# Kernel tuning notes

Measured on AMD Instinct MI355X. Metric: run time of the kernel, lower is better.

Reference implementation:

```python
import jax, jax.numpy as jnp
import numpy as np
from jax import lax

EPS = 1e-6  # LayerNorm2d eps


def _ln2d(x, w, b):
    # channel-wise LayerNorm over dim 1 of [B,C,H,W]
    mu = jnp.mean(x, axis=1, keepdims=True)
    var = jnp.mean((x - mu) ** 2, axis=1, keepdims=True)
    return (x - mu) / jnp.sqrt(var + EPS) * w[None, :, None, None] + b[None, :, None, None]


def _conv1x1(x, w, b):
    # w: [O, C]
    return jnp.einsum('bchw,oc->bohw', x, w) + b[None, :, None, None]


def _dconv(x, w, b):
    # 3x3 conv, dilation 4, padding 4 -> same H,W. w: [O, C, 3, 3]
    y = lax.conv_general_dilated(x, w, window_strides=(1, 1),
                                 padding=((4, 4), (4, 4)), rhs_dilation=(4, 4),
                                 dimension_numbers=('NCHW', 'OIHW', 'NCHW'))
    return y + b[None, :, None, None]


def _forward(x_l, x_r, nl_w, nl_b, nr_w, nr_b, lp1_w, lp1_b, rp1_w, rp1_b,
             dl_w, dl_b, dr_w, dr_b, lp2_w, lp2_b, rp2_w, rp2_b, beta, gamma):
    c = x_l.shape[1]
    scale = c ** (-0.5)
    N_l = _ln2d(x_l, nl_w, nl_b)
    N_r = _ln2d(x_r, nr_w, nr_b)
    V_l = jnp.transpose(_conv1x1(x_l, lp2_w, lp2_b), (0, 2, 3, 1))   # [B,H,W,C]
    V_r = jnp.transpose(_conv1x1(x_r, rp2_w, rp2_b), (0, 2, 3, 1))
    Q_l = jnp.transpose(_conv1x1(N_l, lp1_w, lp1_b), (0, 2, 3, 1))   # [B,H,W,C]
    Q_r = jnp.transpose(_conv1x1(N_r, rp1_w, rp1_b), (0, 2, 3, 1))
    K_l_T = jnp.transpose(_dconv(N_l, dl_w, dl_b), (0, 2, 1, 3))     # [B,H,C,W]
    K_r_T = jnp.transpose(_dconv(N_r, dr_w, dr_b), (0, 2, 1, 3))
    # per-row cross attention: [B,H,W,W]
    attn_r2l = jnp.einsum('bhwc,bhcv->bhwv', Q_l, K_r_T) * scale
    attn_l2r = jnp.einsum('bhwc,bhcv->bhwv', Q_r, K_l_T) * scale
    F_r2l = jnp.einsum('bhwv,bhvc->bhwc', jax.nn.softmax(attn_r2l, axis=-1), V_r)
    F_l2r = jnp.einsum('bhwv,bhvc->bhwc', jax.nn.softmax(attn_l2r, axis=-1), V_l)
    F_r2l = jnp.transpose(F_r2l, (0, 3, 1, 2)) * beta   # [B,C,H,W]
    F_l2r = jnp.transpose(F_l2r, (0, 3, 1, 2)) * gamma
    return x_l + F_r2l, x_r + F_l2r


def setup_inputs() -> dict:
    key = jax.random.key(0)
    ks = jax.random.split(key, 12)
    B, C, H, W = 2, 128, 192, 512
    s = 0.02
    rn = lambda k, shp: s * jax.random.normal(k, shp, jnp.float32)
    return {
        'x_l': jax.random.normal(ks[0], (B, C, H, W), jnp.float32),
        'x_r': jax.random.normal(ks[1], (B, C, H, W), jnp.float32),
        'nl_w': jnp.ones((C,), jnp.float32), 'nl_b': jnp.zeros((C,), jnp.float32),
        'nr_w': jnp.ones((C,), jnp.float32), 'nr_b': jnp.zeros((C,), jnp.float32),
        'lp1_w': rn(ks[2], (C, C)), 'lp1_b': jnp.zeros((C,), jnp.float32),
        'rp1_w': rn(ks[3], (C, C)), 'rp1_b': jnp.zeros((C,), jnp.float32),
        'dl_w': rn(ks[4], (C, C, 3, 3)), 'dl_b': jnp.zeros((C,), jnp.float32),
        'dr_w': rn(ks[5], (C, C, 3, 3)), 'dr_b': jnp.zeros((C,), jnp.float32),
        'lp2_w': rn(ks[6], (C, C)), 'lp2_b': jnp.zeros((C,), jnp.float32),
        'rp2_w': rn(ks[7], (C, C)), 'rp2_b': jnp.zeros((C,), jnp.float32),
        'beta': 0.1 * jax.random.normal(ks[8], (1, C, 1, 1), jnp.float32),
        'gamma': 0.1 * jax.random.normal(ks[9], (1, C, 1, 1), jnp.float32),
    }


def reference(x_l, x_r, nl_w, nl_b, nr_w, nr_b, lp1_w, lp1_b, rp1_w, rp1_b,
              dl_w, dl_b, dr_w, dr_b, lp2_w, lp2_b, rp2_w, rp2_b, beta, gamma):
    return _forward(x_l, x_r, nl_w, nl_b, nr_w, nr_b, lp1_w, lp1_b, rp1_w, rp1_b,
                    dl_w, dl_b, dr_w, dr_b, lp2_w, lp2_b, rp2_w, rp2_b, beta, gamma)
```

## Files before the change

### kernel.cpp

```cpp
#include <hip/hip_runtime.h>
#include <stdint.h>

#define CC 128
#define HH 192
#define WW 512
#define BB 2
#define HW (HH*WW)
#define CHW (CC*HW)
#define TENS (BB*CHW)

typedef __attribute__((ext_vector_type(8))) short bf16x8;
typedef __attribute__((ext_vector_type(4))) short bf16x4;
typedef __attribute__((ext_vector_type(4))) float f32x4;

__device__ __forceinline__ unsigned short f2bf(float f) {
    union { float f; unsigned u; } v; v.f = f;
    return (unsigned short)((v.u + 0x7FFFu + ((v.u >> 16) & 1u)) >> 16);
}
__device__ __forceinline__ float bf2f(unsigned short u) {
    union { unsigned u; float f; } v; v.u = ((unsigned)u) << 16;
    return v.f;
}
__device__ __forceinline__ uint32_t cvtpk(float lo, float hi) {
    uint32_t r;
    asm("v_cvt_pk_bf16_f32 %0, %1, %2" : "=v"(r) : "v"(lo), "v"(hi));
    return r;
}
__device__ __forceinline__ f32x4 MFMA(bf16x8 a, bf16x8 b, f32x4 c) {
    return __builtin_amdgcn_mfma_f32_16x16x32_bf16(a, b, c, 0, 0, 0);
}
__device__ __forceinline__ f32x4 MFMA16(bf16x4 a, bf16x4 b, f32x4 c) {
#if __has_builtin(__builtin_amdgcn_mfma_f32_16x16x16_bf16)
    return __builtin_amdgcn_mfma_f32_16x16x16_bf16(a, b, c, 0, 0, 0);
#elif __has_builtin(__builtin_amdgcn_mfma_f32_16x16x16bf16_1k)
    return __builtin_amdgcn_mfma_f32_16x16x16bf16_1k(a, b, c, 0, 0, 0);
#else
    f32x4 d = c;
    asm("v_mfma_f32_16x16x16_bf16 %0, %1, %2, %0" : "+v"(d) : "v"(a), "v"(b));
    return d;
#endif
}
__device__ __forceinline__ void gload_lds16(const void* g, void* l) {
    __builtin_amdgcn_global_load_lds(
        (const __attribute__((address_space(1))) void*)g,
        (__attribute__((address_space(3))) void*)l, 16, 0, 0);
}

__global__ __launch_bounds__(256) void wcast_k(
    const float* __restrict__ dlw, const float* __restrict__ drw,
    unsigned short* __restrict__ wd)
{
    int i = blockIdx.x * 256 + threadIdx.x;
    if (i >= 2 * 9 * CC * CC) return;
    int e  = i & 7;
    int l  = (i >> 3) & 63;
    int n_ = (i >> 9) & 3;
    int kk = (i >> 11) & 3;
    int oh = (i >> 13) & 1;
    int rest = i >> 14;
    int tap = rest % 9;
    int side = rest / 9;
    int o = oh * 64 + n_ * 16 + (l & 15);
    int c = kk * 32 + (l >> 4) * 8 + e;
    const float* src = side ? drw : dlw;
    wd[i] = f2bf(src[((size_t)o * CC + c) * 9 + tap]);
}

__global__ __launch_bounds__(256) void lnv_k(
    const float* __restrict__ xl, const float* __restrict__ xr,
    const float* __restrict__ nlw, const float* __restrict__ nlb,
    const float* __restrict__ nrw, const float* __restrict__ nrb,
    const float* __restrict__ wlp, const float* __restrict__ blp,
    const float* __restrict__ wrp, const float* __restrict__ brp,
    unsigned short* __restrict__ ntl, unsigned short* __restrict__ ntr,
    unsigned short* __restrict__ vlo, unsigned short* __restrict__ vro)
{
    const int side = blockIdx.y;
    const float* x  = side ? xr : xl;
    const float* nw = side ? nrw : nlw;
    const float* nb = side ? nrb : nlb;
    const float* wv = side ? wrp : wlp;
    const float* bv = side ? brp : blp;
    unsigned short* nt = side ? ntr : ntl;
    unsigned short* vo = side ? vro : vlo;
    const int bid = blockIdx.x;
    const int wt = bid & 7, h = (bid >> 3) % HH, b = bid / (8 * HH);
    const int w0 = wt * 64;
    const int t = threadIdx.x;

    __shared__ unsigned short sA[64][136];
    __shared__ unsigned short sB[128][136];
    __shared__ float red[8][64];
    __shared__ float smu[64], srs[64];

    {
        const int w = t & 63, cg = t >> 6;
        const float* xp = x + (size_t)b * CHW + (size_t)h * WW + w0 + w;
        float s = 0.f, q = 0.f;
        for (int i = 0; i < 16; i++) {
            int c = cg * 32 + i * 2;
            float v0 = xp[(size_t)c * HW];
            float v1 = xp[(size_t)(c + 1) * HW];
            *(uint32_t*)&sA[w][c] = cvtpk(v0, v1);
            s += v0 + v1; q += v0 * v0 + v1 * v1;
        }
        red[cg][w] = s; red[4 + cg][w] = q;
    }
    for (int it = 0; it < 16; it++) {
        int f = it * 1024 + t * 4;
        int o = f >> 7, c = f & 127;
        float4 v = *(const float4*)(wv + o * CC + c);
        *(uint32_t*)&sB[o][c]     = cvtpk(v.x, v.y);
        *(uint32_t*)&sB[o][c + 2] = cvtpk(v.z, v.w);
    }
    __syncthreads();
    if (t < 64) {
        float S = red[0][t] + red[1][t] + red[2][t] + red[3][t];
        float Q = red[4][t] + red[5][t] + red[6][t] + red[7][t];
        float mu = S * (1.f / CC);
        float var = fmaxf(Q * (1.f / CC) - mu * mu, 0.f);
        smu[t] = mu; srs[t] = rsqrtf(var + 1e-6f);
    }
    __syncthreads();
    {
        const int cl = (t & 63) * 2, wg = t >> 6;
        const float nwa = nw[cl], nwb = nw[cl + 1];
        const float nba = nb[cl], nbb = nb[cl + 1];
        unsigned short* npb = nt + ((size_t)(b * HH + h) * WW + w0) * CC;
        for (int wp = 0; wp < 16; wp++) {
            int w = wp * 4 + wg;
            float mu = smu[w], rs = srs[w];
            float v0 = (bf2f(sA[w][cl]) - mu) * rs * nwa + nba;
            float v1 = (bf2f(sA[w][cl + 1]) - mu) * rs * nwb + nbb;
            *(uint32_t*)&npb[(size_t)w * CC + cl] = cvtpk(v0, v1);
        }
    }
    const int wid = t >> 6, l = t & 63, lr = l & 15, lg = l >> 4;
    f32x4 acc[8] = {};
    for (int kk = 0; kk < 4; kk++) {
        bf16x8 a = *(const bf16x8*)&sA[wid * 16 + lr][kk * 32 + lg * 8];
#pragma unroll
        for (int n_ = 0; n_ < 8; n_++) {
            bf16x8 bb = *(const bf16x8*)&sB[n_ * 16 + lr][kk * 32 + lg * 8];
            acc[n_] = MFMA(a, bb, acc[n_]);
        }
    }
    unsigned short* vp = vo + ((size_t)(b * HH + h) * CC) * WW + w0;
    for (int n_ = 0; n_ < 8; n_++) {
        int o = n_ * 16 + lr;
        float bias = bv[o];
        uint2 uu;
        uu.x = cvtpk(acc[n_][0] + bias, acc[n_][1] + bias);
        uu.y = cvtpk(acc[n_][2] + bias, acc[n_][3] + bias);
        *(uint2*)&vp[(size_t)o * WW + wid * 16 + lg * 4] = uu;
    }
}

__global__ __launch_bounds__(256) void dconv_k(
    const unsigned short* __restrict__ ntl, const unsigned short* __restrict__ ntr,
    const unsigned short* __restrict__ wfr,
    const float* __restrict__ dlb, const float* __restrict__ drb,
    unsigned short* __restrict__ klo, unsigned short* __restrict__ kro)
{
    const int side = blockIdx.y;
    const unsigned short* nt = side ? ntr : ntl;
    const unsigned short* wbase = wfr + (size_t)side * 9 * 16384;
    const float* bd = side ? drb : dlb;
    unsigned short* ko = side ? kro : klo;
    const int bid0 = blockIdx.x;
    const int lgc = (bid0 & 7) * 192 + (bid0 >> 3);
    const int wt = lgc & 3;
    const int hb = lgc >> 2;
    const int h = hb % HH, b = hb / HH;
    const int w0 = wt * 128;
    const int t = threadIdx.x;
    const int wid = t >> 6, l = t & 63, lr = l & 15, lg = l >> 4;
    const int whalf = wid & 1, ohalf = wid >> 1;

    __shared__ unsigned short sA[136][136];

    f32x4 acc[4][4] = {};
    for (int dy = 0; dy < 3; dy++) {
        const int hh = h + 4 * (dy - 1);
        const bool hok = (hh >= 0 && hh < HH);
        __syncthreads();
        for (int f = t * 8; f < 136 * 128; f += 2048) {
            int wloc = f >> 7, c = f & 127;
            int w = w0 - 4 + wloc;
            bf16x8 v = {0, 0, 0, 0, 0, 0, 0, 0};
            if (hok && w >= 0 && w < WW)
                v = *(const bf16x8*)(nt + ((size_t)(b * HH + hh) * WW + w) * CC + c);
            *(bf16x8*)&sA[wloc][c] = v;
        }
        __syncthreads();
#pragma unroll
        for (int dx = 0; dx < 3; dx++) {
            const unsigned short* wtap =
                wbase + (size_t)(dy * 3 + dx) * 16384 + ohalf * 8192 + l * 8;
#pragma unroll
            for (int kk = 0; kk < 4; kk++) {
                bf16x8 bfr[4];
#pragma unroll
                for (int n_ = 0; n_ < 4; n_++)
                    bfr[n_] = *(const bf16x8*)(wtap + (kk * 4 + n_) * 512);
                bf16x8 af[4];
#pragma unroll
                for (int g = 0; g < 4; g++)
                    af[g] = *(const bf16x8*)&sA[whalf * 64 + g * 16 + lr + 4 * dx][kk * 32 + lg * 8];
#pragma unroll
                for (int g = 0; g < 4; g++)
#pragma unroll
                    for (int n_ = 0; n_ < 4; n_++)
                        acc[g][n_] = MFMA(af[g], bfr[n_], acc[g][n_]);
            }
        }
    }
    unsigned short* kp = ko + ((size_t)(b * HH + h) * WW + w0) * CC;
    for (int g = 0; g < 4; g++)
        for (int n_ = 0; n_ < 4; n_++) {
            int o = ohalf * 64 + n_ * 16 + lr;
            float bias = bd[o];
            for (int j = 0; j < 4; j++) {
                int w = whalf * 64 + g * 16 + lg * 4 + j;
                kp[(size_t)w * CC + o] = f2bf(acc[g][n_][j] + bias);
            }
        }
}

__global__ __launch_bounds__(256, 3) void attn_k(
    const unsigned short* __restrict__ ntl, const unsigned short* __restrict__ ntr,
    const unsigned short* __restrict__ kl,  const unsigned short* __restrict__ kr,
    const unsigned short* __restrict__ vtl, const unsigned short* __restrict__ vtr,
    const float* __restrict__ lp1w, const float* __restrict__ lp1b,
    const float* __restrict__ rp1w, const float* __restrict__ rp1b,
    const float* __restrict__ xl, const float* __restrict__ xr,
    const float* __restrict__ beta, const float* __restrict__ gamma,
    float* __restrict__ out)
{
    __shared__ __align__(16) char smem[52224];
    unsigned short* sQ  = (unsigned short*)smem;
    unsigned short* sWh = (unsigned short*)(smem + 34816);

    const int dir = blockIdx.z;
    const unsigned short* nq  = dir ? ntr : ntl;
    const unsigned short* kws = dir ? kl : kr;
    const unsigned short* vws = dir ? vtl : vtr;
    const float* wq   = dir ? rp1w : lp1w;
    const float* bq   = dir ? rp1b : lp1b;
    const float* xres = dir ? xr : xl;
    const float* mult = dir ? gamma : beta;
    float* op = out + (size_t)dir * TENS;

    const int bid = blockIdx.x;
    const int xcd = bid & 7;
    const int s   = bid >> 3;
    const int qb  = s & 3;
    const int bh  = xcd + 8 * (s >> 2);
    const int q0  = qb * 128;
    const int t = threadIdx.x;
    const int wid = t >> 6, l = t & 63, lr = l & 15, lg = l >> 4;

    const unsigned short* ksrc = kws + (size_t)bh * WW * CC;
    const unsigned short* vsrc = vws + (size_t)bh * CC * WW;

    int koff[4], voff[4];
#pragma unroll
    for (int it = 0; it < 4; it++) {
        int row = it * 16 + wid * 4 + (l >> 4);
        int gci = (l & 15) ^ (row & 7);
        koff[it] = row * CC + gci * 8;
    }
#pragma unroll
    for (int it = 0; it < 4; it++) {
        int row = it * 32 + wid * 8 + (l >> 3);
        int gci = (l & 7) ^ (row & 7);
        voff[it] = row * WW + gci * 8;
    }

    {
        const unsigned short* nsrc = nq + ((size_t)bh * WW + q0) * CC;
        for (int it = 0; it < 8; it++) {
            int f = it * 2048 + t * 8;
            *(bf16x8*)&sQ[(f >> 7) * 136 + (f & 127)] = *(const bf16x8*)(nsrc + f);
        }
        for (int it = 0; it < 8; it++) {
            int f = it * 1024 + t * 4;
            int o = f >> 7, c = f & 127;
            float4 v = *(const float4*)(wq + o * CC + c);
            *(uint32_t*)&sWh[o * 136 + c]     = cvtpk(v.x, v.y);
            *(uint32_t*)&sWh[o * 136 + c + 2] = cvtpk(v.z, v.w);
        }
    }
    f32x4 qacc[2][8] = {};
    __syncthreads();
    for (int kk = 0; kk < 4; kk++) {
        bf16x8 a0 = *(const bf16x8*)&sQ[(wid * 32 + lr) * 136 + kk * 32 + lg * 8];
        bf16x8 a1 = *(const bf16x8*)&sQ[(wid * 32 + 16 + lr) * 136 + kk * 32 + lg * 8];
#pragma unroll
        for (int n_ = 0; n_ < 4; n_++) {
            bf16x8 b = *(const bf16x8*)&sWh[(n_ * 16 + lr) * 136 + kk * 32 + lg * 8];
            qacc[0][n_] = MFMA(a0, b, qacc[0][n_]);
            qacc[1][n_] = MFMA(a1, b, qacc[1][n_]);
        }
    }
    __syncthreads();
    for (int it = 0; it < 8; it++) {
        int f = it * 1024 + t * 4;
        int o = f >> 7, c = f & 127;
        float4 v = *(const float4*)(wq + (o + 64) * CC + c);
        *(uint32_t*)&sWh[o * 136 + c]     = cvtpk(v.x, v.y);
        *(uint32_t*)&sWh[o * 136 + c + 2] = cvtpk(v.z, v.w);
    }
    __syncthreads();
    for (int kk = 0; kk < 4; kk++) {
        bf16x8 a0 = *(const bf16x8*)&sQ[(wid * 32 + lr) * 136 + kk * 32 + lg * 8];
        bf16x8 a1 = *(const bf16x8*)&sQ[(wid * 32 + 16 + lr) * 136 + kk * 32 + lg * 8];
#pragma unroll
        for (int n_ = 0; n_ < 4; n_++) {
            bf16x8 b = *(const bf16x8*)&sWh[(n_ * 16 + lr) * 136 + kk * 32 + lg * 8];
            qacc[0][4 + n_] = MFMA(a0, b, qacc[0][4 + n_]);
            qacc[1][4 + n_] = MFMA(a1, b, qacc[1][4 + n_]);
        }
    }
    __syncthreads();
    {
        const float SCL = 0.08838834764831845f * 1.4426950408889634f;
#pragma unroll
        for (int mg = 0; mg < 2; mg++)
#pragma unroll
            for (int n_ = 0; n_ < 8; n_++) {
                float bias = bq[n_ * 16 + lr];
#pragma unroll
                for (int j = 0; j < 4; j++)
                    sQ[(wid * 32 + mg * 16 + lg * 4 + j) * 136 + n_ * 16 + lr] =
                        f2bf((qacc[mg][n_][j] + bias) * SCL);
            }
    }
    __syncthreads();
    bf16x8 qf[2][4];
#pragma unroll
    for (int qg = 0; qg < 2; qg++)
#pragma unroll
        for (int kk = 0; kk < 4; kk++)
            qf[qg][kk] = *(const bf16x8*)&sQ[(wid * 32 + qg * 16 + lr) * 136 + kk * 32 + lg * 8];

    f32x4 oacc[8][2] = {};
    float mrow[2] = {-1e30f, -1e30f};
    float lrow[2] = {0.f, 0.f};
    const int lr7 = lr & 7;

    for (int kb = 0; kb < 8; kb++) {
        __syncthreads();
        {
            const unsigned short* kS = ksrc + kb * 64 * CC;
            const unsigned short* vS = vsrc + kb * 64;
#pragma unroll
            for (int it = 0; it < 4; it++)
                gload_lds16(kS + koff[it], smem + it * 4096 + wid * 1024);
#pragma unroll
            for (int it = 0; it < 4; it++)
                gload_lds16(vS + voff[it], smem + 16384 + it * 4096 + wid * 1024);
        }
        __syncthreads();
        f32x4 sacc[2][4] = {};
        __builtin_amdgcn_s_setprio(1);
        for (int kk = 0; kk < 4; kk++)
#pragma unroll
            for (int n_ = 0; n_ < 4; n_++) {
                bf16x8 kf = *(const bf16x8*)(smem + (n_ * 16 + lr) * 256
                                             + (((kk * 4 + lg) ^ lr7) << 4));
                sacc[0][n_] = MFMA(kf, qf[0][kk], sacc[0][n_]);
                sacc[1][n_] = MFMA(kf, qf[1][kk], sacc[1][n_]);
            }
        __builtin_amdgcn_s_setprio(0);
        float pm[2];
#pragma unroll
        for (int qg = 0; qg < 2; qg++) {
            float m_ = sacc[qg][0][0];
#pragma unroll
            for (int n_ = 0; n_ < 4; n_++)
#pragma unroll
                for (int j = 0; j < 4; j++) m_ = fmaxf(m_, sacc[qg][n_][j]);
            m_ = fmaxf(m_, __shfl_xor(m_, 16, 64));
            m_ = fmaxf(m_, __shfl_xor(m_, 32, 64));
            pm[qg] = m_;
        }
        bool need = (pm[0] - mrow[0] > 8.f) || (pm[1] - mrow[1] > 8.f);
        if (__any(need)) {
            float al[2];
#pragma unroll
            for (int qg = 0; qg < 2; qg++) {
                float mn = fmaxf(mrow[qg], pm[qg]);
                al[qg] = exp2f(mrow[qg] - mn);
                mrow[qg] = mn;
                lrow[qg] *= al[qg];
            }
#pragma unroll
            for (int n_ = 0; n_ < 8; n_++)
#pragma unroll
                for (int qg = 0; qg < 2; qg++) {
                    f32x4 o = oacc[n_][qg];
                    o[0] *= al[qg]; o[1] *= al[qg]; o[2] *= al[qg]; o[3] *= al[qg];
                    oacc[n_][qg] = o;
                }
        }
#pragma unroll
        for (int qg = 0; qg < 2; qg++) {
            float rs = 0.f;
#pragma unroll
            for (int n_ = 0; n_ < 4; n_++)
#pragma unroll
                for (int j = 0; j < 4; j++) {
                    float e = exp2f(sacc[qg][n_][j] - mrow[qg]);
                    sacc[qg][n_][j] = e;
                    rs += e;
                }
            rs += __shfl_xor(rs, 16, 64);
            rs += __shfl_xor(rs, 32, 64);
            lrow[qg] += rs;
        }
        __builtin_amdgcn_s_setprio(1);
#pragma unroll
        for (int n_ = 0; n_ < 4; n_++) {
            union { uint32_t u[2]; bf16x4 v; } b0, b1;
            b0.u[0] = cvtpk(sacc[0][n_][0], sacc[0][n_][1]);
            b0.u[1] = cvtpk(sacc[0][n_][2], sacc[0][n_][3]);
            b1.u[0] = cvtpk(sacc[1][n_][0], sacc[1][n_][1]);
            b1.u[1] = cvtpk(sacc[1][n_][2], sacc[1][n_][3]);
#pragma unroll
            for (int n8 = 0; n8 < 8; n8++) {
                bf16x4 va = *(const bf16x4*)(smem + 16384 + (n8 * 16 + lr) * 128
                                             + ((((n_ * 2) + (lg >> 1)) ^ lr7) << 4)
                                             + ((lg & 1) << 3));
                oacc[n8][0] = MFMA16(va, b0.v, oacc[n8][0]);
                oacc[n8][1] = MFMA16(va, b1.v, oacc[n8][1]);
            }
        }
        __builtin_amdgcn_s_setprio(0);
    }

    const float inv0 = 1.f / lrow[0], inv1 = 1.f / lrow[1];
    const int b = bh / HH, h = bh % HH;
    const int w_0 = q0 + wid * 32 + lr;
    const float* xp0 = xres + (size_t)b * CHW + (size_t)h * WW + w_0;
    float* outp0 = op + (size_t)b * CHW + (size_t)h * WW + w_0;
#pragma unroll
    for (int n_ = 0; n_ < 8; n_++) {
        float4 m4 = *(const float4*)&mult[n_ * 16 + lg * 4];
#pragma unroll
        for (int j = 0; j < 4; j++) {
            int c = n_ * 16 + lg * 4 + j;
            float mj = (&m4.x)[j];
            outp0[(size_t)c * HW]      = xp0[(size_t)c * HW]      + oacc[n_][0][j] * inv0 * mj;
            outp0[(size_t)c * HW + 16] = xp0[(size_t)c * HW + 16] + oacc[n_][1][j] * inv1 * mj;
        }
    }
}

extern "C" void kernel_launch(void* const* d_in, const int* in_sizes, int n_in,
                              void* d_out, int out_size, void* d_ws, size_t ws_size,
                              hipStream_t stream)
{
    const float* xl   = (const float*)d_in[0];
    const float* xr   = (const float*)d_in[1];
    const float* nlw  = (const float*)d_in[2];
    const float* nlb  = (const float*)d_in[3];
    const float* nrw  = (const float*)d_in[4];
    const float* nrb  = (const float*)d_in[5];
    const float* lp1w = (const float*)d_in[6];
    const float* lp1b = (const float*)d_in[7];
    const float* rp1w = (const float*)d_in[8];
    const float* rp1b = (const float*)d_in[9];
    const float* dlw  = (const float*)d_in[10];
    const float* dlb  = (const float*)d_in[11];
    const float* drw  = (const float*)d_in[12];
    const float* drb  = (const float*)d_in[13];
    const float* lp2w = (const float*)d_in[14];
    const float* lp2b = (const float*)d_in[15];
    const float* rp2w = (const float*)d_in[16];
    const float* rp2b = (const float*)d_in[17];
    const float* beta = (const float*)d_in[18];
    const float* gamma= (const float*)d_in[19];
    float* out = (float*)d_out;

    unsigned short* ws = (unsigned short*)d_ws;
    const size_t A = (size_t)TENS;
    unsigned short* Ntl = ws;
    unsigned short* Ntr = ws + A;
    unsigned short* Kl  = ws + 2 * A;
    unsigned short* Kr  = ws + 3 * A;
    unsigned short* Vtl = ws + 4 * A;
    unsigned short* Vtr = ws + 5 * A;
    unsigned short* Wd  = ws + 6 * A;

    wcast_k<<<dim3(1152), 256, 0, stream>>>(dlw, drw, Wd);
    lnv_k<<<dim3(3072, 2), 256, 0, stream>>>(xl, xr, nlw, nlb, nrw, nrb,
        lp2w, lp2b, rp2w, rp2b, Ntl, Ntr, Vtl, Vtr);
    dconv_k<<<dim3(1536, 2), 256, 0, stream>>>(Ntl, Ntr, Wd, dlb, drb, Kl, Kr);
    attn_k<<<dim3(1536, 1, 2), 256, 0, stream>>>(Ntl, Ntr, Kl, Kr, Vtl, Vtr,
        lp1w, lp1b, rp1w, rp1b, xl, xr, beta, gamma, out);
}
```

Before: 523.3 us.

## Move Q projection from attention kernel into LayerNorm/V-projection kernel

Computes the scaled Q projection inside lnv_k, reusing the normalized tile already in shared memory, and writes Q to a new workspace buffer. The attention kernel then loads precomputed Q fragments straight from global memory, dropping its weight staging, the two MFMA passes and several barriers. Its shared memory falls from 52 KB to 32 KB, which may allow more resident blocks. The cost is an extra bf16 Q tensor written and read through global memory, plus more work and LDS traffic in lnv_k.

```diff
diff --git a/kernel.cpp b/kernel.cpp
--- a/kernel.cpp
+++ b/kernel.cpp
@@ -72,8 +72,11 @@
     const float* __restrict__ nrw, const float* __restrict__ nrb,
     const float* __restrict__ wlp, const float* __restrict__ blp,
     const float* __restrict__ wrp, const float* __restrict__ brp,
+    const float* __restrict__ wlq, const float* __restrict__ blq,
+    const float* __restrict__ wrq, const float* __restrict__ brq,
     unsigned short* __restrict__ ntl, unsigned short* __restrict__ ntr,
-    unsigned short* __restrict__ vlo, unsigned short* __restrict__ vro)
+    unsigned short* __restrict__ vlo, unsigned short* __restrict__ vro,
+    unsigned short* __restrict__ qlo, unsigned short* __restrict__ qro)
 {
     const int side = blockIdx.y;
     const float* x  = side ? xr : xl;
@@ -81,12 +84,16 @@
     const float* nb = side ? nrb : nlb;
     const float* wv = side ? wrp : wlp;
     const float* bv = side ? brp : blp;
+    const float* wq = side ? wrq : wlq;
+    const float* bq = side ? brq : blq;
     unsigned short* nt = side ? ntr : ntl;
     unsigned short* vo = side ? vro : vlo;
+    unsigned short* qo = side ? qro : qlo;
     const int bid = blockIdx.x;
     const int wt = bid & 7, h = (bid >> 3) % HH, b = bid / (8 * HH);
     const int w0 = wt * 64;
     const int t = threadIdx.x;
+    const int wid = t >> 6, l = t & 63, lr = l & 15, lg = l >> 4;
 
     __shared__ unsigned short sA[64][136];
     __shared__ unsigned short sB[128][136];
@@ -135,7 +142,6 @@
             *(uint32_t*)&npb[(size_t)w * CC + cl] = cvtpk(v0, v1);
         }
     }
-    const int wid = t >> 6, l = t & 63, lr = l & 15, lg = l >> 4;
     f32x4 acc[8] = {};
     for (int kk = 0; kk < 4; kk++) {
         bf16x8 a = *(const bf16x8*)&sA[wid * 16 + lr][kk * 32 + lg * 8];
@@ -153,6 +159,51 @@
         uu.x = cvtpk(acc[n_][0] + bias, acc[n_][1] + bias);
         uu.y = cvtpk(acc[n_][2] + bias, acc[n_][3] + bias);
         *(uint2*)&vp[(size_t)o * WW + wid * 16 + lg * 4] = uu;
+    }
+    __syncthreads();
+    {
+        const int w = wid * 16 + (l >> 2), c0 = (l & 3) * 32;
+        const float mu = smu[w], rs = srs[w];
+        for (int i = 0; i < 32; i += 2) {
+            int c = c0 + i;
+            float v0 = (bf2f(sA[w][c]) - mu) * rs * nw[c] + nb[c];
+            float v1 = (bf2f(sA[w][c + 1]) - mu) * rs * nw[c + 1] + nb[c + 1];
+            *(uint32_t*)&sA[w][c] = cvtpk(v0, v1);
+        }
+    }
+    for (int it = 0; it < 16; it++) {
+        int f = it * 1024 + t * 4;
+        int o = f >> 7, c = f & 127;
+        float4 v = *(const float4*)(wq + o * CC + c);
+        *(uint32_t*)&sB[o][c]     = cvtpk(v.x, v.y);
+        *(uint32_t*)&sB[o][c + 2] = cvtpk(v.z, v.w);
+    }
+    __syncthreads();
+    f32x4 qa[8] = {};
+    for (int kk = 0; kk < 4; kk++) {
+        bf16x8 a = *(const bf16x8*)&sA[wid * 16 + lr][kk * 32 + lg * 8];
+#pragma unroll
+        for (int n_ = 0; n_ < 8; n_++) {
+            bf16x8 bb = *(const bf16x8*)&sB[n_ * 16 + lr][kk * 32 + lg * 8];
+            qa[n_] = MFMA(a, bb, qa[n_]);
+        }
+    }
+    const float SCL = 0.08838834764831845f * 1.4426950408889634f;
+    for (int n_ = 0; n_ < 8; n_++) {
+        int o = n_ * 16 + lr;
+        float bias = bq[o];
+#pragma unroll
+        for (int j = 0; j < 4; j++)
+            sA[wid * 16 + lg * 4 + j][o] = f2bf((qa[n_][j] + bias) * SCL);
+    }
+    {
+        unsigned short* qp = qo + ((size_t)(b * HH + h) * WW + w0 + wid * 16) * CC;
+#pragma unroll
+        for (int r = 0; r < 4; r++) {
+            int row = r * 4 + (l >> 4);
+            int col = (l & 15) * 8;
+            *(bf16x8*)&qp[row * CC + col] = *(const bf16x8*)&sA[wid * 16 + row][col];
+        }
     }
 }
 
@@ -228,25 +279,19 @@
 }
 
 __global__ __launch_bounds__(256, 3) void attn_k(
-    const unsigned short* __restrict__ ntl, const unsigned short* __restrict__ ntr,
+    const unsigned short* __restrict__ qsl, const unsigned short* __restrict__ qsr,
     const unsigned short* __restrict__ kl,  const unsigned short* __restrict__ kr,
     const unsigned short* __restrict__ vtl, const unsigned short* __restrict__ vtr,
-    const float* __restrict__ lp1w, const float* __restrict__ lp1b,
-    const float* __restrict__ rp1w, const float* __restrict__ rp1b,
     const float* __restrict__ xl, const float* __restrict__ xr,
     const float* __restrict__ beta, const float* __restrict__ gamma,
     float* __restrict__ out)
 {
-    __shared__ __align__(16) char smem[52224];
-    unsigned short* sQ  = (unsigned short*)smem;
-    unsigned short* sWh = (unsigned short*)(smem + 34816);
+    __shared__ __align__(16) char smem[32768];
 
     const int dir = blockIdx.z;
-    const unsigned short* nq  = dir ? ntr : ntl;
+    const unsigned short* qws = dir ? qsr : qsl;
     const unsigned short* kws = dir ? kl : kr;
     const unsigned short* vws = dir ? vtl : vtr;
-    const float* wq   = dir ? rp1w : lp1w;
-    const float* bq   = dir ? rp1b : lp1b;
     const float* xres = dir ? xr : xl;
     const float* mult = dir ? gamma : beta;
     float* op = out + (size_t)dir * TENS;
@@ -263,6 +308,17 @@
     const unsigned short* ksrc = kws + (size_t)bh * WW * CC;
     const unsigned short* vsrc = vws + (size_t)bh * CC * WW;
 
+    bf16x8 qf[2][4];
+    {
+        const unsigned short* qsrc = qws + ((size_t)bh * WW + q0) * CC;
+#pragma unroll
+        for (int qg = 0; qg < 2; qg++)
+#pragma unroll
+            for (int kk = 0; kk < 4; kk++)
+                qf[qg][kk] = *(const bf16x8*)(qsrc + (wid * 32 + qg * 16 + lr) * CC
+                                              + kk * 32 + lg * 8);
+    }
+
     int koff[4], voff[4];
 #pragma unroll
     for (int it = 0; it < 4; it++) {
@@ -276,73 +332,6 @@
         int gci = (l & 7) ^ (row & 7);
         voff[it] = row * WW + gci * 8;
     }
-
-    {
-        const unsigned short* nsrc = nq + ((size_t)bh * WW + q0) * CC;
-        for (int it = 0; it < 8; it++) {
-            int f = it * 2048 + t * 8;
-            *(bf16x8*)&sQ[(f >> 7) * 136 + (f & 127)] = *(const bf16x8*)(nsrc + f);
-        }
-        for (int it = 0; it < 8; it++) {
-            int f = it * 1024 + t * 4;
-            int o = f >> 7, c = f & 127;
-            float4 v = *(const float4*)(wq + o * CC + c);
-            *(uint32_t*)&sWh[o * 136 + c]     = cvtpk(v.x, v.y);
-            *(uint32_t*)&sWh[o * 136 + c + 2] = cvtpk(v.z, v.w);
-        }
-    }
-    f32x4 qacc[2][8] = {};
-    __syncthreads();
-    for (int kk = 0; kk < 4; kk++) {
-        bf16x8 a0 = *(const bf16x8*)&sQ[(wid * 32 + lr) * 136 + kk * 32 + lg * 8];
-        bf16x8 a1 = *(const bf16x8*)&sQ[(wid * 32 + 16 + lr) * 136 + kk * 32 + lg * 8];
-#pragma unroll
-        for (int n_ = 0; n_ < 4; n_++) {
-            bf16x8 b = *(const bf16x8*)&sWh[(n_ * 16 + lr) * 136 + kk * 32 + lg * 8];
-            qacc[0][n_] = MFMA(a0, b, qacc[0][n_]);
-            qacc[1][n_] = MFMA(a1, b, qacc[1][n_]);
-        }
-    }
-    __syncthreads();
-    for (int it = 0; it < 8; it++) {
-        int f = it * 1024 + t * 4;
-        int o = f >> 7, c = f & 127;
-        float4 v = *(const float4*)(wq + (o + 64) * CC + c);
-        *(uint32_t*)&sWh[o * 136 + c]     = cvtpk(v.x, v.y);
-        *(uint32_t*)&sWh[o * 136 + c + 2] = cvtpk(v.z, v.w);
-    }
-    __syncthreads();
-    for (int kk = 0; kk < 4; kk++) {
-        bf16x8 a0 = *(const bf16x8*)&sQ[(wid * 32 + lr) * 136 + kk * 32 + lg * 8];
-        bf16x8 a1 = *(const bf16x8*)&sQ[(wid * 32 + 16 + lr) * 136 + kk * 32 + lg * 8];
-#pragma unroll
-        for (int n_ = 0; n_ < 4; n_++) {
-            bf16x8 b = *(const bf16x8*)&sWh[(n_ * 16 + lr) * 136 + kk * 32 + lg * 8];
-            qacc[0][4 + n_] = MFMA(a0, b, qacc[0][4 + n_]);
-            qacc[1][4 + n_] = MFMA(a1, b, qacc[1][4 + n_]);
-        }
-    }
-    __syncthreads();
-    {
-        const float SCL = 0.08838834764831845f * 1.4426950408889634f;
-#pragma unroll
-        for (int mg = 0; mg < 2; mg++)
-#pragma unroll
-            for (int n_ = 0; n_ < 8; n_++) {
-                float bias = bq[n_ * 16 + lr];
-#pragma unroll
-                for (int j = 0; j < 4; j++)
-                    sQ[(wid * 32 + mg * 16 + lg * 4 + j) * 136 + n_ * 16 + lr] =
-                        f2bf((qacc[mg][n_][j] + bias) * SCL);
-            }
-    }
-    __syncthreads();
-    bf16x8 qf[2][4];
-#pragma unroll
-    for (int qg = 0; qg < 2; qg++)
-#pragma unroll
-        for (int kk = 0; kk < 4; kk++)
-            qf[qg][kk] = *(const bf16x8*)&sQ[(wid * 32 + qg * 16 + lr) * 136 + kk * 32 + lg * 8];
 
     f32x4 oacc[8][2] = {};
     float mrow[2] = {-1e30f, -1e30f};
@@ -491,12 +480,15 @@
     unsigned short* Kr  = ws + 3 * A;
     unsigned short* Vtl = ws + 4 * A;
     unsigned short* Vtr = ws + 5 * A;
-    unsigned short* Wd  = ws + 6 * A;
+    unsigned short* Qsl = ws + 6 * A;
+    unsigned short* Qsr = ws + 7 * A;
+    unsigned short* Wd  = ws + 8 * A;
 
     wcast_k<<<dim3(1152), 256, 0, stream>>>(dlw, drw, Wd);
     lnv_k<<<dim3(3072, 2), 256, 0, stream>>>(xl, xr, nlw, nlb, nrw, nrb,
-        lp2w, lp2b, rp2w, rp2b, Ntl, Ntr, Vtl, Vtr);
+        lp2w, lp2b, rp2w, rp2b, lp1w, lp1b, rp1w, rp1b,
+        Ntl, Ntr, Vtl, Vtr, Qsl, Qsr);
     dconv_k<<<dim3(1536, 2), 256, 0, stream>>>(Ntl, Ntr, Wd, dlb, drb, Kl, Kr);
-    attn_k<<<dim3(1536, 1, 2), 256, 0, stream>>>(Ntl, Ntr, Kl, Kr, Vtl, Vtr,
-        lp1w, lp1b, rp1w, rp1b, xl, xr, beta, gamma, out);
-}
+    attn_k<<<dim3(1536, 1, 2), 256, 0, stream>>>(Qsl, Qsr, Kl, Kr, Vtl, Vtr,
+        xl, xr, beta, gamma, out);
+}
```

New measurement: 578.5 us. 10.6% more time.

## Keep projected Q in registers as MFMA B-operand fragments, drop sQ staging

Applied to the files above, without the earlier changes.

The Q projection now computes W·N^T directly, so its accumulator layout matches the B-operand fragment of the 16x16x16 MFMA used in the QK^T score computation. The projected, scaled Q therefore stays in registers and is no longer written to and read back from LDS. This removes the sQ buffer, shrinking LDS from 52KB to 32KB, which could allow more resident blocks, and it removes several barriers. The trade-offs are that the score loop switches from K=32 MFMAs to twice as many K=16 MFMAs with narrower LDS reads, and N is loaded straight from global memory into registers.

```diff
diff --git a/kernel.cpp b/kernel.cpp
--- a/kernel.cpp
+++ b/kernel.cpp
@@ -237,9 +237,8 @@
     const float* __restrict__ beta, const float* __restrict__ gamma,
     float* __restrict__ out)
 {
-    __shared__ __align__(16) char smem[52224];
-    unsigned short* sQ  = (unsigned short*)smem;
-    unsigned short* sWh = (unsigned short*)(smem + 34816);
+    __shared__ __align__(16) char smem[32768];
+    unsigned short* sWh = (unsigned short*)smem;
 
     const int dir = blockIdx.z;
     const unsigned short* nq  = dir ? ntr : ntl;
@@ -263,6 +262,51 @@
     const unsigned short* ksrc = kws + (size_t)bh * WW * CC;
     const unsigned short* vsrc = vws + (size_t)bh * CC * WW;
 
+    bf16x8 nf[2][4];
+    {
+        const unsigned short* nsrc = nq + ((size_t)bh * WW + q0) * CC;
+#pragma unroll
+        for (int qg = 0; qg < 2; qg++)
+#pragma unroll
+            for (int kk = 0; kk < 4; kk++)
+                nf[qg][kk] = *(const bf16x8*)(nsrc + (wid * 32 + qg * 16 + lr) * CC
+                                              + kk * 32 + lg * 8);
+    }
+
+    const float SCL = 0.08838834764831845f * 1.4426950408889634f;
+    uint2 qfb[8][2];
+#pragma unroll
+    for (int h_ = 0; h_ < 2; h_++) {
+        if (h_) __syncthreads();
+        for (int it = 0; it < 8; it++) {
+            int f = it * 1024 + t * 4;
+            int o = f >> 7, c = f & 127;
+            float4 v = *(const float4*)(wq + (h_ * 64 + o) * CC + c);
+            *(uint32_t*)&sWh[o * 136 + c]     = cvtpk(v.x, v.y);
+            *(uint32_t*)&sWh[o * 136 + c + 2] = cvtpk(v.z, v.w);
+        }
+        __syncthreads();
+#pragma unroll
+        for (int n4 = 0; n4 < 4; n4++) {
+            bf16x8 wqA[4];
+#pragma unroll
+            for (int kk = 0; kk < 4; kk++)
+                wqA[kk] = *(const bf16x8*)&sWh[(n4 * 16 + lr) * 136 + kk * 32 + lg * 8];
+            f32x4 qa0 = {}, qa1 = {};
+#pragma unroll
+            for (int kk = 0; kk < 4; kk++) {
+                qa0 = MFMA(wqA[kk], nf[0][kk], qa0);
+                qa1 = MFMA(wqA[kk], nf[1][kk], qa1);
+            }
+            int n_ = h_ * 4 + n4;
+            float4 b4 = *(const float4*)(bq + n_ * 16 + lg * 4);
+            qfb[n_][0].x = cvtpk((qa0[0] + b4.x) * SCL, (qa0[1] + b4.y) * SCL);
+            qfb[n_][0].y = cvtpk((qa0[2] + b4.z) * SCL, (qa0[3] + b4.w) * SCL);
+            qfb[n_][1].x = cvtpk((qa1[0] + b4.x) * SCL, (qa1[1] + b4.y) * SCL);
+            qfb[n_][1].y = cvtpk((qa1[2] + b4.z) * SCL, (qa1[3] + b4.w) * SCL);
+        }
+    }
+
     int koff[4], voff[4];
 #pragma unroll
     for (int it = 0; it < 4; it++) {
@@ -276,73 +320,6 @@
         int gci = (l & 7) ^ (row & 7);
         voff[it] = row * WW + gci * 8;
     }
-
-    {
-        const unsigned short* nsrc = nq + ((size_t)bh * WW + q0) * CC;
-        for (int it = 0; it < 8; it++) {
-            int f = it * 2048 + t * 8;
-            *(bf16x8*)&sQ[(f >> 7) * 136 + (f & 127)] = *(const bf16x8*)(nsrc + f);
-        }
-        for (int it = 0; it < 8; it++) {
-            int f = it * 1024 + t * 4;
-            int o = f >> 7, c = f & 127;
-            float4 v = *(const float4*)(wq + o * CC + c);
-            *(uint32_t*)&sWh[o * 136 + c]     = cvtpk(v.x, v.y);
-            *(uint32_t*)&sWh[o * 136 + c + 2] = cvtpk(v.z, v.w);
-        }
-    }
-    f32x4 qacc[2][8] = {};
-    __syncthreads();
-    for (int kk = 0; kk < 4; kk++) {
-        bf16x8 a0 = *(const bf16x8*)&sQ[(wid * 32 + lr) * 136 + kk * 32 + lg * 8];
-        bf16x8 a1 = *(const bf16x8*)&sQ[(wid * 32 + 16 + lr) * 136 + kk * 32 + lg * 8];
-#pragma unroll
-        for (int n_ = 0; n_ < 4; n_++) {
-            bf16x8 b = *(const bf16x8*)&sWh[(n_ * 16 + lr) * 136 + kk * 32 + lg * 8];
-            qacc[0][n_] = MFMA(a0, b, qacc[0][n_]);
-            qacc[1][n_] = MFMA(a1, b, qacc[1][n_]);
-        }
-    }
-    __syncthreads();
-    for (int it = 0; it < 8; it++) {
-        int f = it * 1024 + t * 4;
-        int o = f >> 7, c = f & 127;
-        float4 v = *(const float4*)(wq + (o + 64) * CC + c);
-        *(uint32_t*)&sWh[o * 136 + c]     = cvtpk(v.x, v.y);
-        *(uint32_t*)&sWh[o * 136 + c + 2] = cvtpk(v.z, v.w);
-    }
-    __syncthreads();
-    for (int kk = 0; kk < 4; kk++) {
-        bf16x8 a0 = *(const bf16x8*)&sQ[(wid * 32 + lr) * 136 + kk * 32 + lg * 8];
-        bf16x8 a1 = *(const bf16x8*)&sQ[(wid * 32 + 16 + lr) * 136 + kk * 32 + lg * 8];
-#pragma unroll
-        for (int n_ = 0; n_ < 4; n_++) {
-            bf16x8 b = *(const bf16x8*)&sWh[(n_ * 16 + lr) * 136 + kk * 32 + lg * 8];
-            qacc[0][4 + n_] = MFMA(a0, b, qacc[0][4 + n_]);
-            qacc[1][4 + n_] = MFMA(a1, b, qacc[1][4 + n_]);
-        }
-    }
-    __syncthreads();
-    {
-        const float SCL = 0.08838834764831845f * 1.4426950408889634f;
-#pragma unroll
-        for (int mg = 0; mg < 2; mg++)
-#pragma unroll
-            for (int n_ = 0; n_ < 8; n_++) {
-                float bias = bq[n_ * 16 + lr];
-#pragma unroll
-                for (int j = 0; j < 4; j++)
-                    sQ[(wid * 32 + mg * 16 + lg * 4 + j) * 136 + n_ * 16 + lr] =
-                        f2bf((qacc[mg][n_][j] + bias) * SCL);
-            }
-    }
-    __syncthreads();
-    bf16x8 qf[2][4];
-#pragma unroll
-    for (int qg = 0; qg < 2; qg++)
-#pragma unroll
-        for (int kk = 0; kk < 4; kk++)
-            qf[qg][kk] = *(const bf16x8*)&sQ[(wid * 32 + qg * 16 + lr) * 136 + kk * 32 + lg * 8];
 
     f32x4 oacc[8][2] = {};
     float mrow[2] = {-1e30f, -1e30f};
@@ -364,14 +341,17 @@
         __syncthreads();
         f32x4 sacc[2][4] = {};
         __builtin_amdgcn_s_setprio(1);
-        for (int kk = 0; kk < 4; kk++)
-#pragma unroll
-            for (int n_ = 0; n_ < 4; n_++) {
-                bf16x8 kf = *(const bf16x8*)(smem + (n_ * 16 + lr) * 256
-                                             + (((kk * 4 + lg) ^ lr7) << 4));
-                sacc[0][n_] = MFMA(kf, qf[0][kk], sacc[0][n_]);
-                sacc[1][n_] = MFMA(kf, qf[1][kk], sacc[1][n_]);
-            }
+#pragma unroll
+        for (int n4 = 0; n4 < 4; n4++) {
+#pragma unroll
+            for (int s_ = 0; s_ < 8; s_++) {
+                bf16x4 ka = *(const bf16x4*)(smem + (n4 * 16 + lr) * 256
+                                             + ((((s_ * 2) + (lg >> 1)) ^ lr7) << 4)
+                                             + ((lg & 1) << 3));
+                sacc[0][n4] = MFMA16(ka, *(const bf16x4*)&qfb[s_][0], sacc[0][n4]);
+                sacc[1][n4] = MFMA16(ka, *(const bf16x4*)&qfb[s_][1], sacc[1][n4]);
+            }
+        }
         __builtin_amdgcn_s_setprio(0);
         float pm[2];
 #pragma unroll
```

Measured after the change: 672.3 us. 1.28x slower.
